# Optimization experiments

Measured on AMD Instinct MI355X. Metric: run time of the kernel, lower is better.

## Reference

```python
import jax, jax.numpy as jnp
import numpy as np

B, T, U, V = 16, 128, 64, 1024
BLANK = 0
NEG = -1e30  # safe -inf surrogate for fp32


def _combine(a, b):
    # log-semiring affine recurrence composition: alpha[u] = logaddexp(c[u], alpha[u-1] + e[u])
    e1, c1 = a
    e2, c2 = b
    return (e1 + e2, jnp.logaddexp(c2, c1 + e2))


def rnnt_loss_mean(acts, labels):
    # acts: [B,T,U,V] raw logits; labels: [B,U-1] int
    lp = jax.nn.log_softmax(acts, axis=-1)          # [B,T,U,V]
    lp_blank = lp[..., BLANK]                        # [B,T,U]
    # lp_label[b,t,u] = lp[b,t,u,labels[b,u]], u in [0,U-2]
    lp_label = jnp.take_along_axis(
        lp[:, :, : U - 1, :], labels[:, None, :, None].astype(jnp.int32), axis=-1
    )[..., 0]                                        # [B,T,U-1]

    b = acts.shape[0]
    dt = lp.dtype
    # row t=0: alpha[0,u] = cumsum of label log-probs
    alpha0 = jnp.concatenate(
        [jnp.zeros((b, 1), dt), jnp.cumsum(lp_label[:, 0, :], axis=-1)], axis=-1
    )                                                # [B,U]

    def step(alpha_prev, inputs):
        lpb_prev, lpl_t = inputs                     # [B,U], [B,U-1]
        c = alpha_prev + lpb_prev                    # blank transition from row t-1
        e = jnp.concatenate([jnp.full((b, 1), NEG, dt), lpl_t], axis=-1)
        _, alpha = jax.lax.associative_scan(_combine, (e, c), axis=-1)
        return alpha, None

    xs = (
        jnp.moveaxis(lp_blank[:, :-1, :], 1, 0),     # [T-1,B,U]
        jnp.moveaxis(lp_label[:, 1:, :], 1, 0),      # [T-1,B,U-1]
    )
    alpha_last, _ = jax.lax.scan(step, alpha0, xs)   # alpha at t=T-1: [B,U]
    loglike = alpha_last[:, -1] + lp_blank[:, -1, -1]
    costs = -loglike                                 # [B]
    # reduction='mean': sum then divide by batch, keep shape [1] like unsqueeze(-1)
    return (jnp.sum(costs) / b)[None]


def setup_inputs() -> dict:
    key = jax.random.key(0)
    k1, k2 = jax.random.split(key)
    acts = jax.random.normal(k1, (B, T, U, V), dtype=jnp.float32)
    labels = jax.random.randint(k2, (B, U - 1), 0, V, dtype=jnp.int32)
    act_lens = jnp.full((B,), T, dtype=jnp.int32)
    label_lens = jnp.full((B,), U - 1, dtype=jnp.int32)
    return {"acts": acts, "labels": labels, "act_lens": act_lens, "label_lens": label_lens}


def reference(acts, labels, act_lens, label_lens):
    # act_lens/label_lens are full (T, U-1) per certify_inputs max constraints
    return rnnt_loss_mean(acts, labels)
```

## Files before the change

kernel.cpp:

```cpp
#include <hip/hip_runtime.h>

#define B_ 16
#define T_ 128
#define U_ 64
#define V_ 1024
#define NDIAG (T_ + U_ - 1)
#define NEG (-1e30f)

__device__ __forceinline__ float lae(float a, float b) {
    float mx = fmaxf(a, b);
    float mn = fminf(a, b);
    return mx + __logf(1.f + __expf(mn - mx));
}

__global__ __launch_bounds__(256) void lsm_kernel(
    const float* __restrict__ acts, const int* __restrict__ labels,
    float* __restrict__ lpb_d, float* __restrict__ lpl_d, float* __restrict__ out)
{
    if (blockIdx.x == 0 && threadIdx.x == 0) out[0] = 0.f;

    const int lane = threadIdx.x & 63;
    const int row  = (blockIdx.x << 2) + (threadIdx.x >> 6);
    const float4* p4 = reinterpret_cast<const float4*>(acts + (size_t)row * V_);

    float4 v0 = p4[lane];
    float4 v1 = p4[64 + lane];
    float4 v2 = p4[128 + lane];
    float4 v3 = p4[192 + lane];

    float s = __expf(v0.x) + __expf(v0.y) + __expf(v0.z) + __expf(v0.w)
            + __expf(v1.x) + __expf(v1.y) + __expf(v1.z) + __expf(v1.w)
            + __expf(v2.x) + __expf(v2.y) + __expf(v2.z) + __expf(v2.w)
            + __expf(v3.x) + __expf(v3.y) + __expf(v3.z) + __expf(v3.w);
    #pragma unroll
    for (int d = 32; d >= 1; d >>= 1) s += __shfl_xor(s, d, 64);
    const float lse = __logf(s);

    const int b  = row >> 13;
    const int tu = row & 8191;
    const int u  = tu & 63;
    const int dg = (tu >> 6) + u;

    float lab = 0.f;
    if (u < U_ - 1) {
        const int l     = labels[b * (U_ - 1) + u];
        const int chunk = l >> 8, src = (l >> 2) & 63, comp = l & 3;
        float4 vc  = (chunk == 0) ? v0 : (chunk == 1) ? v1 : (chunk == 2) ? v2 : v3;
        float cand = (comp == 0) ? vc.x : (comp == 1) ? vc.y : (comp == 2) ? vc.z : vc.w;
        lab = __shfl(cand, src, 64);
    }

    if (lane == 0) {
        const size_t o = ((size_t)b * NDIAG + dg) * U_ + u;
        lpb_d[o] = v0.x - lse;
        if (u < U_ - 1) lpl_d[o] = lab - lse;
    }
}

__global__ __launch_bounds__(64) void alpha_kernel(
    const float* __restrict__ lpb_d, const float* __restrict__ lpl_d,
    float* __restrict__ out)
{
    const int b = blockIdx.x;
    const int u = threadIdx.x;
    const size_t base = (size_t)b * NDIAG * U_;
    const int j = (u == 0) ? 0 : u - 1;

    float pb = lpb_d[base + u];
    float pl = lpl_d[base + j];

    float alpha = (u == 0) ? 0.f : NEG;

    for (int d = 1; d < NDIAG; ++d) {
        float pb_n = lpb_d[base + (size_t)d * U_ + u];
        float pl_n = lpl_d[base + (size_t)d * U_ + j];

        const int t = d - u;
        const float left  = __shfl_up(alpha, 1, 64);
        const float blank = (t >= 1 && t <= T_ - 1) ? alpha + pb : NEG;
        const float labl  = (u >= 1 && t >= 0 && t <= T_ - 1) ? left + pl : NEG;
        const float a_new = lae(blank, labl);
        alpha = (t >= 0 && t <= T_ - 1) ? a_new : NEG;

        pb = pb_n; pl = pl_n;
    }
    if (u == 63) {
        const float loglike = alpha + pb;
        atomicAdd(out, -loglike * (1.f / B_));
    }
}

extern "C" void kernel_launch(void* const* d_in, const int* in_sizes, int n_in,
                              void* d_out, int out_size, void* d_ws, size_t ws_size,
                              hipStream_t stream)
{
    const float* acts   = (const float*)d_in[0];
    const int*   labels = (const int*)d_in[1];
    float* out = (float*)d_out;

    float* lpb_d = (float*)d_ws;
    float* lpl_d = lpb_d + (size_t)B_ * NDIAG * U_;

    const int rows = B_ * T_ * U_;
    lsm_kernel<<<rows / 4, 256, 0, stream>>>(acts, labels, lpb_d, lpl_d, out);
    alpha_kernel<<<B_, 64, 0, stream>>>(lpb_d, lpl_d, out);
}
```

Measured before the change: 717.7 us.

## Warp-specialize alpha kernel with double-buffered LDS prefetch of diagonal chunks

The alpha recurrence kernel now runs 256 threads per batch. One wavefront computes the diagonal recurrence out of shared memory while the other three prefetch the next chunk of 28 diagonals into a double buffer. The left-neighbor shuffle is replaced with a DPP row-shift intrinsic. This targets the global-load latency on the serial 190-step dependency chain, at the cost of a block barrier per chunk and more LDS use. The DPP row shift (0x138) may not match a full 64-lane shift, so alpha could be wrong at lane boundaries.

```diff
diff --git a/kernel.cpp b/kernel.cpp
--- a/kernel.cpp
+++ b/kernel.cpp
@@ -6,6 +6,9 @@
 #define V_ 1024
 #define NDIAG (T_ + U_ - 1)
 #define NEG (-1e30f)
+
+#define CH 28
+#define NPH ((NDIAG + CH - 1) / CH)
 
 __device__ __forceinline__ float lae(float a, float b) {
     float mx = fmaxf(a, b);
@@ -57,35 +60,73 @@
     }
 }
 
-__global__ __launch_bounds__(64) void alpha_kernel(
+__global__ __launch_bounds__(256) void alpha_kernel(
     const float* __restrict__ lpb_d, const float* __restrict__ lpl_d,
     float* __restrict__ out)
 {
-    const int b = blockIdx.x;
-    const int u = threadIdx.x;
+    __shared__ float s_pb[2][CH][U_];
+    __shared__ float s_pl[2][CH][U_];
+
+    const int b   = blockIdx.x;
+    const int tid = threadIdx.x;
     const size_t base = (size_t)b * NDIAG * U_;
+
+    {
+        const int cnt4 = CH * U_ / 4;
+        const float4* sb = reinterpret_cast<const float4*>(lpb_d + base);
+        const float4* sl = reinterpret_cast<const float4*>(lpl_d + base);
+        float4* db = reinterpret_cast<float4*>(&s_pb[0][0][0]);
+        float4* dl = reinterpret_cast<float4*>(&s_pl[0][0][0]);
+        for (int i = tid; i < cnt4; i += 256) { db[i] = sb[i]; dl[i] = sl[i]; }
+    }
+    __syncthreads();
+
+    const int u = tid & 63;
     const int j = (u == 0) ? 0 : u - 1;
+    float alpha  = (u == 0) ? 0.f : NEG;
+    float lastpb = 0.f;
 
-    float pb = lpb_d[base + u];
-    float pl = lpl_d[base + j];
+    for (int p = 0; p < NPH; ++p) {
+        if (tid >= 64) {
+            const int g0 = (p + 1) * CH;
+            if (g0 < NDIAG) {
+                const int nd   = min(CH, NDIAG - g0);
+                const int cnt4 = nd * U_ / 4;
+                const float4* sb = reinterpret_cast<const float4*>(lpb_d + base + (size_t)g0 * U_);
+                const float4* sl = reinterpret_cast<const float4*>(lpl_d + base + (size_t)g0 * U_);
+                float4* db = reinterpret_cast<float4*>(&s_pb[(p + 1) & 1][0][0]);
+                float4* dl = reinterpret_cast<float4*>(&s_pl[(p + 1) & 1][0][0]);
+                for (int i = tid - 64; i < cnt4; i += 192) { db[i] = sb[i]; dl[i] = sl[i]; }
+            }
+        } else {
+            const int g0 = p * CH;
+            const int ge = min(g0 + CH, NDIAG);
+            #pragma unroll
+            for (int k = 0; k < CH; ++k) {
+                const int g = g0 + k;
+                if (g >= ge) break;
+                const float pb = s_pb[p & 1][k][u];
+                if (g < NDIAG - 1) {
+                    const float pl = s_pl[p & 1][k][j];
+                    const int d = g + 1;
+                    const int t = d - u;
+                    const float left = __int_as_float(__builtin_amdgcn_update_dpp(
+                        __float_as_int(alpha), __float_as_int(alpha),
+                        0x138 , 0xf, 0xf, false));
+                    const float blank = (t >= 1 && t <= T_ - 1) ? alpha + pb : NEG;
+                    const float labl  = (u >= 1 && t >= 0 && t <= T_ - 1) ? left + pl : NEG;
+                    const float a_new = lae(blank, labl);
+                    alpha = (t >= 0 && t <= T_ - 1) ? a_new : NEG;
+                } else {
+                    lastpb = pb;
+                }
+            }
+        }
+        __syncthreads();
+    }
 
-    float alpha = (u == 0) ? 0.f : NEG;
-
-    for (int d = 1; d < NDIAG; ++d) {
-        float pb_n = lpb_d[base + (size_t)d * U_ + u];
-        float pl_n = lpl_d[base + (size_t)d * U_ + j];
-
-        const int t = d - u;
-        const float left  = __shfl_up(alpha, 1, 64);
-        const float blank = (t >= 1 && t <= T_ - 1) ? alpha + pb : NEG;
-        const float labl  = (u >= 1 && t >= 0 && t <= T_ - 1) ? left + pl : NEG;
-        const float a_new = lae(blank, labl);
-        alpha = (t >= 0 && t <= T_ - 1) ? a_new : NEG;
-
-        pb = pb_n; pl = pl_n;
-    }
-    if (u == 63) {
-        const float loglike = alpha + pb;
+    if (tid == 63) {
+        const float loglike = alpha + lastpb;
         atomicAdd(out, -loglike * (1.f / B_));
     }
 }
@@ -103,5 +144,5 @@
 
     const int rows = B_ * T_ * U_;
     lsm_kernel<<<rows / 4, 256, 0, stream>>>(acts, labels, lpb_d, lpl_d, out);
-    alpha_kernel<<<B_, 64, 0, stream>>>(lpb_d, lpl_d, out);
+    alpha_kernel<<<B_, 256, 0, stream>>>(lpb_d, lpl_d, out);
 }
```

After: 682.6 us, median of 2. 1.05x faster.
